# Kernel optimization log

Hardware: AMD Instinct MI355X
Metric: run time of the kernel (lower is better)

Reference implementation:

```python
import jax, jax.numpy as jnp
import numpy as np

N = 65536        # nodes
E = 131072       # directed edges
D = 512          # emb_dim
L = 5            # num_layer
G = 512          # num graphs
EPS = 1e-5       # batchnorm eps
NUM_ATOM_TYPE, NUM_CHIRALITY = 120, 3
NUM_BOND_TYPE, NUM_BOND_DIR = 6, 3


def setup_inputs() -> dict:
    key = jax.random.key(0)
    ks = jax.random.split(key, 12)
    s = 0.02
    return {
        "x": jax.random.randint(ks[0], (N, 2), 0, 3),
        "edge_index": jax.random.randint(ks[1], (2, E), 0, N),
        "edge_attr": jax.random.randint(ks[2], (E, 2), 0, 3),
        "batch": jnp.sort(jax.random.randint(ks[3], (N,), 0, G)),
        "x_emb1": jax.random.normal(ks[4], (NUM_ATOM_TYPE, D), jnp.float32) * s,
        "x_emb2": jax.random.normal(ks[5], (NUM_CHIRALITY, D), jnp.float32) * s,
        "e_emb1": jax.random.normal(ks[6], (L, NUM_BOND_TYPE, D), jnp.float32) * s,
        "e_emb2": jax.random.normal(ks[7], (L, NUM_BOND_DIR, D), jnp.float32) * s,
        "W1": jax.random.normal(ks[8], (L, D, 2 * D), jnp.float32) * s,
        "b1": jnp.zeros((L, 2 * D), jnp.float32),
        "W2": jax.random.normal(ks[9], (L, 2 * D, D), jnp.float32) * s,
        "b2": jnp.zeros((L, D), jnp.float32),
        "gamma": jnp.ones((L, D), jnp.float32),
        "beta": jnp.zeros((L, D), jnp.float32),
    }


def reference(x, edge_index, edge_attr, batch,
              x_emb1, x_emb2, e_emb1, e_emb2,
              W1, b1, W2, b2, gamma, beta):
    n = x.shape[0]
    # atom embedding: type + chirality
    h = x_emb1[x[:, 0]] + x_emb2[x[:, 1]]                     # [N, D]

    # add self loops (appended after real edges, attr = [4, 0])
    loops = jnp.arange(n)
    src = jnp.concatenate([edge_index[0], loops])             # [E+N]
    dst = jnp.concatenate([edge_index[1], loops])
    sl_attr = jnp.concatenate(
        [jnp.full((n, 1), 4, dtype=edge_attr.dtype),
         jnp.zeros((n, 1), dtype=edge_attr.dtype)], axis=1)
    ea = jnp.concatenate([edge_attr, sl_attr], axis=0)        # [E+N, 2]

    for l in range(L):
        # per-edge embedding: bond type + bond direction
        e = e_emb1[l][ea[:, 0]] + e_emb2[l][ea[:, 1]]         # [E+N, D]
        msg = h[src] + e                                      # gather + add
        agg = jax.ops.segment_sum(msg, dst, num_segments=n)   # scatter-add
        # GIN MLP: Linear(D,2D) -> ReLU -> Linear(2D,D)
        hh = jax.nn.relu(agg @ W1[l] + b1[l]) @ W2[l] + b2[l]
        # BatchNorm1d (training-mode batch statistics)
        mean = hh.mean(axis=0)
        var = hh.var(axis=0)
        hh = (hh - mean) * jax.lax.rsqrt(var + EPS) * gamma[l] + beta[l]
        if l < L - 1:
            hh = jax.nn.relu(hh)   # dropout(p=0) is identity
        h = hh

    # JK='last': node rep = h; graph rep = global mean pool over batch ids
    counts = jax.ops.segment_sum(jnp.ones((n,), h.dtype), batch, num_segments=G)
    graph = jax.ops.segment_sum(h, batch, num_segments=G) / jnp.maximum(counts, 1.0)[:, None]
    return graph, h
```

## Files before the change

### kernel.cpp

```cpp
#include <hip/hip_runtime.h>
#include <stdint.h>

#define Nn 65536
#define Ee 131072
#define Dd 512
#define D2 1024
#define Ll 5
#define Gg 512
#define EPSf 1e-5f

typedef __bf16 bf16x8 __attribute__((ext_vector_type(8)));
typedef float f32x4 __attribute__((ext_vector_type(4)));

__device__ __forceinline__ unsigned short f2bf(float f) {
    union { float f; unsigned u; } c; c.f = f;
    unsigned r = c.u + 0x7fffu + ((c.u >> 16) & 1u);
    return (unsigned short)(r >> 16);
}

__device__ __forceinline__ void add4(float4& a, float4 b) {
    a.x += b.x; a.y += b.y; a.z += b.z; a.w += b.w;
}

__device__ __forceinline__ void gload_lds16(const void* g, void* l) {
    __builtin_amdgcn_global_load_lds(
        (const __attribute__((address_space(1))) void*)(uintptr_t)g,
        (__attribute__((address_space(3))) void*)(unsigned)(uintptr_t)l,
        16, 0, 0);
}

__global__ void k_transW(const float* __restrict__ src, unsigned short* __restrict__ dst,
                         int K, int Nw) {
    long total = (long)Ll * K * Nw;
    for (long idx = (long)blockIdx.x * blockDim.x + threadIdx.x; idx < total;
         idx += (long)gridDim.x * blockDim.x) {
        long l = idx / ((long)K * Nw);
        long rem = idx - l * (long)K * Nw;
        int k = (int)(rem / Nw), n = (int)(rem % Nw);
        dst[(l * Nw + n) * K + k] = f2bf(src[idx]);
    }
}

__global__ void k_embed(const int* __restrict__ x,
                        const float4* __restrict__ xe1, const float4* __restrict__ xe2,
                        float4* __restrict__ h4) {
    const int total = Nn * 128;
    for (int idx = blockIdx.x * blockDim.x + threadIdx.x; idx < total;
         idx += gridDim.x * blockDim.x) {
        int node = idx >> 7, c = idx & 127;
        int t0 = x[2 * node], t1 = x[2 * node + 1];
        float4 v = xe1[t0 * 128 + c];
        float4 w = xe2[t1 * 128 + c];
        v.x += w.x; v.y += w.y; v.z += w.z; v.w += w.w;
        h4[idx] = v;
    }
}

__global__ void k_zeroN(int* __restrict__ p, int n) {
    int i = blockIdx.x * blockDim.x + threadIdx.x;
    if (i < n) p[i] = 0;
}

__global__ void k_hist(const int* __restrict__ edst, int* __restrict__ cnt) {
    int e = blockIdx.x * blockDim.x + threadIdx.x;
    if (e < Ee) atomicAdd(&cnt[edst[e]], 1);
}

__global__ void k_scan(const int* __restrict__ cnt, int* __restrict__ off,
                       int* __restrict__ cursor) {
    __shared__ int part[1024];
    int t = threadIdx.x;
    int base = t * 64;
    int s = 0;
    for (int i = 0; i < 64; ++i) s += cnt[base + i];
    part[t] = s;
    __syncthreads();
    for (int d = 1; d < 1024; d <<= 1) {
        int v = (t >= d) ? part[t - d] : 0;
        __syncthreads();
        part[t] += v;
        __syncthreads();
    }
    int run = part[t] - s;
    for (int i = 0; i < 64; ++i) {
        off[base + i] = run;
        cursor[base + i] = run;
        run += cnt[base + i];
    }
    if (t == 1023) off[Nn] = run;
}

__global__ void k_place(const int* __restrict__ esrc, const int* __restrict__ edst,
                        const int* __restrict__ eattr, int* __restrict__ cursor,
                        int* __restrict__ csrc, int* __restrict__ cattr) {
    int e = blockIdx.x * blockDim.x + threadIdx.x;
    if (e < Ee) {
        int d = edst[e];
        int p = atomicAdd(&cursor[d], 1);
        csrc[p] = esrc[e];
        cattr[p] = eattr[2 * e] * 3 + eattr[2 * e + 1];
    }
}

template <int NORM>
__global__ __launch_bounds__(256) void k_gather(const float* __restrict__ hin,
                                                const float* __restrict__ ss,
                                                const int* __restrict__ off,
                                                const int* __restrict__ csrc,
                                                const int* __restrict__ cattr,
                                                const float* __restrict__ e1l,
                                                const float* __restrict__ e2l,
                                                unsigned short* __restrict__ aggb) {
    int node = (blockIdx.x << 2) + (threadIdx.x >> 6);
    int lane = threadIdx.x & 63;
    int c0 = lane, c1 = lane + 64;
    float4 sa0, sb0, sa1, sb1;
    if (NORM) {
        const float4* ss4 = (const float4*)ss;
        sa0 = ss4[c0]; sb0 = ss4[128 + c0];
        sa1 = ss4[c1]; sb1 = ss4[128 + c1];
    }
    auto loadrow = [&](const float4* row, int c, float4 a, float4 b) -> float4 {
        float4 v = row[c];
        if (NORM) {
            v.x = fmaxf(fmaf(v.x, a.x, b.x), 0.f);
            v.y = fmaxf(fmaf(v.y, a.y, b.y), 0.f);
            v.z = fmaxf(fmaf(v.z, a.z, b.z), 0.f);
            v.w = fmaxf(fmaf(v.w, a.w, b.w), 0.f);
        }
        return v;
    };
    const float4* hn = (const float4*)(hin + (size_t)node * Dd);
    const float4* s1 = (const float4*)(e1l + 4 * Dd);
    const float4* s2 = (const float4*)(e2l);
    float4 A0 = loadrow(hn, c0, sa0, sb0);
    float4 A1 = loadrow(hn, c1, sa1, sb1);
    add4(A0, s1[c0]); add4(A0, s2[c0]);
    add4(A1, s1[c1]); add4(A1, s2[c1]);
    int kb = off[node], ke = off[node + 1];
    for (int k = kb; k < ke; ++k) {
        int s = csrc[k];
        int at = cattr[k];
        const float4* hs = (const float4*)(hin + (size_t)s * Dd);
        const float4* p1 = (const float4*)(e1l + (size_t)(at / 3) * Dd);
        const float4* p2 = (const float4*)(e2l + (size_t)(at % 3) * Dd);
        add4(A0, loadrow(hs, c0, sa0, sb0)); add4(A0, p1[c0]); add4(A0, p2[c0]);
        add4(A1, loadrow(hs, c1, sa1, sb1)); add4(A1, p1[c1]); add4(A1, p2[c1]);
    }
    unsigned short* dst = aggb + (size_t)node * Dd;
    ushort4 o0, o1;
    o0.x = f2bf(A0.x); o0.y = f2bf(A0.y); o0.z = f2bf(A0.z); o0.w = f2bf(A0.w);
    o1.x = f2bf(A1.x); o1.y = f2bf(A1.y); o1.z = f2bf(A1.z); o1.w = f2bf(A1.w);
    *(ushort4*)(dst + c0 * 4) = o0;
    *(ushort4*)(dst + c1 * 4) = o1;
}

__device__ __forceinline__ void stage_q(const unsigned short* __restrict__ g, int ldk,
                                        long row0, int col0, char* region, int tid) {
    int wbase = (tid >> 6) << 10;
#pragma unroll
    for (int r = 0; r < 2; ++r) {
        int gi = tid + r * 512;
        int row = gi >> 2;
        int k16 = (gi & 3) ^ ((row >> 1) & 3);
        gload_lds16(g + (row0 + row) * (long)ldk + col0 + k16 * 8,
                    region + r * 8192 + wbase);
    }
}

__device__ __forceinline__ bf16x8 rd_frag(const char* region, int row, int l4) {
    int slot = l4 ^ ((row >> 1) & 3);
    return *(const bf16x8*)(region + row * 64 + (slot << 4));
}

template <int EPI>
__global__ __launch_bounds__(512, 2) void gemm8(const unsigned short* __restrict__ A,
                                                const unsigned short* __restrict__ BT,
                                                const float* __restrict__ bias,
                                                unsigned short* __restrict__ Cb,
                                                float* __restrict__ Cf,
                                                float* __restrict__ stats,
                                                int M, int N, int K) {
    __shared__ __align__(16) char lds[131072];
    const int tid = threadIdx.x;
    const int lane = tid & 63;
    const int w = tid >> 6;
    const int wm = w >> 2, wn = w & 3;
    const int l15 = lane & 15, l4 = lane >> 4;

    const int nwg = gridDim.x;
    const int cpx = nwg >> 3;
    const int bid = blockIdx.x;
    const int wg = (bid & 7) * cpx + (bid >> 3);
    const int ntn = N >> 8;
    const long bm = (long)(wg / ntn) * 256;
    const long bn = (long)(wg % ntn) * 256;

    char* Ab = lds;
    char* Bb = lds + 65536;
    const int NT = K >> 6;

    f32x4 acc[8][4];
#pragma unroll
    for (int i = 0; i < 8; ++i)
#pragma unroll
        for (int j = 0; j < 4; ++j) acc[i][j] = (f32x4){0.f, 0.f, 0.f, 0.f};

    stage_q(A, K, bm, 0, Ab, tid);
    stage_q(BT, K, bn, 0, Bb, tid);
    stage_q(A, K, bm, 32, Ab + 16384, tid);
    stage_q(BT, K, bn, 32, Bb + 16384, tid);
    if (NT > 1) {
        stage_q(A, K, bm, 64, Ab + 32768, tid);
        stage_q(BT, K, bn, 64, Bb + 32768, tid);
    }
    asm volatile("s_waitcnt vmcnt(4)" ::: "memory");
    __builtin_amdgcn_s_barrier();

    for (int t = 0; t < NT; ++t) {
        const int cur = t & 1;
        char* Acur = Ab + cur * 32768;
        char* Bcur = Bb + cur * 32768;
        char* Anxt = Ab + (cur ^ 1) * 32768;
        char* Bnxt = Bb + (cur ^ 1) * 32768;
        bf16x8 af[8], bv[2];

#pragma unroll
        for (int fm = 0; fm < 8; ++fm)
            af[fm] = rd_frag(Acur, wm * 128 + fm * 16 + l15, l4);
#pragma unroll
        for (int fn = 0; fn < 2; ++fn)
            bv[fn] = rd_frag(Bcur, wn * 64 + fn * 16 + l15, l4);
        if (t + 1 < NT) stage_q(A, K, bm, (t + 1) * 64 + 32, Anxt + 16384, tid);
        __builtin_amdgcn_s_barrier();
        asm volatile("s_waitcnt lgkmcnt(0)" ::: "memory");
        __builtin_amdgcn_s_setprio(1);
#pragma unroll
        for (int fm = 0; fm < 8; ++fm)
#pragma unroll
            for (int fn = 0; fn < 2; ++fn)
                acc[fm][fn] = __builtin_amdgcn_mfma_f32_16x16x32_bf16(af[fm], bv[fn], acc[fm][fn], 0, 0, 0);
        __builtin_amdgcn_s_setprio(0);
        __builtin_amdgcn_s_barrier();

#pragma unroll
        for (int fn = 0; fn < 2; ++fn)
            bv[fn] = rd_frag(Bcur, wn * 64 + 32 + fn * 16 + l15, l4);
        if (t + 1 < NT) stage_q(BT, K, bn, (t + 1) * 64 + 32, Bnxt + 16384, tid);
        __builtin_amdgcn_s_barrier();
        asm volatile("s_waitcnt lgkmcnt(0)" ::: "memory");
        __builtin_amdgcn_s_setprio(1);
#pragma unroll
        for (int fm = 0; fm < 8; ++fm)
#pragma unroll
            for (int fn = 0; fn < 2; ++fn)
                acc[fm][2 + fn] = __builtin_amdgcn_mfma_f32_16x16x32_bf16(af[fm], bv[fn], acc[fm][2 + fn], 0, 0, 0);
        __builtin_amdgcn_s_setprio(0);
        __builtin_amdgcn_s_barrier();

#pragma unroll
        for (int fm = 0; fm < 8; ++fm)
            af[fm] = rd_frag(Acur + 16384, wm * 128 + fm * 16 + l15, l4);
#pragma unroll
        for (int fn = 0; fn < 2; ++fn)
            bv[fn] = rd_frag(Bcur + 16384, wn * 64 + fn * 16 + l15, l4);
        if (t + 2 < NT) stage_q(A, K, bm, (t + 2) * 64, Acur, tid);
        __builtin_amdgcn_s_barrier();
        asm volatile("s_waitcnt lgkmcnt(0)" ::: "memory");
        __builtin_amdgcn_s_setprio(1);
#pragma unroll
        for (int fm = 0; fm < 8; ++fm)
#pragma unroll
            for (int fn = 0; fn < 2; ++fn)
                acc[fm][fn] = __builtin_amdgcn_mfma_f32_16x16x32_bf16(af[fm], bv[fn], acc[fm][fn], 0, 0, 0);
        __builtin_amdgcn_s_setprio(0);
        __builtin_amdgcn_s_barrier();

#pragma unroll
        for (int fn = 0; fn < 2; ++fn)
            bv[fn] = rd_frag(Bcur + 16384, wn * 64 + 32 + fn * 16 + l15, l4);
        if (t + 2 < NT) stage_q(BT, K, bn, (t + 2) * 64, Bcur, tid);
        __builtin_amdgcn_s_barrier();
        asm volatile("s_waitcnt lgkmcnt(0)" ::: "memory");
        __builtin_amdgcn_s_setprio(1);
#pragma unroll
        for (int fm = 0; fm < 8; ++fm)
#pragma unroll
            for (int fn = 0; fn < 2; ++fn)
                acc[fm][2 + fn] = __builtin_amdgcn_mfma_f32_16x16x32_bf16(af[fm], bv[fn], acc[fm][2 + fn], 0, 0, 0);
        __builtin_amdgcn_s_setprio(0);
        if (t + 2 < NT) {
            asm volatile("s_waitcnt vmcnt(4)" ::: "memory");
        } else if (t + 1 < NT) {
            asm volatile("s_waitcnt vmcnt(0)" ::: "memory");
        }
        __builtin_amdgcn_s_barrier();
    }

    const long row_base = bm + wm * 128;
    const int col_base = (int)bn + wn * 64;
    float cs[4] = {0.f, 0.f, 0.f, 0.f}, cq[4] = {0.f, 0.f, 0.f, 0.f};
#pragma unroll
    for (int fn = 0; fn < 4; ++fn) {
        int col = col_base + fn * 16 + l15;
        float bval = bias[col];
#pragma unroll
        for (int fm = 0; fm < 8; ++fm) {
            long row0 = row_base + fm * 16 + l4 * 4;
#pragma unroll
            for (int r = 0; r < 4; ++r) {
                float v = acc[fm][fn][r] + bval;
                if (EPI == 0) {
                    v = fmaxf(v, 0.f);
                    Cb[(row0 + r) * N + col] = f2bf(v);
                } else {
                    Cf[(row0 + r) * N + col] = v;
                    cs[fn] += v;
                    cq[fn] += v * v;
                }
            }
        }
    }
    if (EPI == 1) {
#pragma unroll
        for (int fn = 0; fn < 4; ++fn) {
            float s = cs[fn], q = cq[fn];
            s += __shfl_xor(s, 16); s += __shfl_xor(s, 32);
            q += __shfl_xor(q, 16); q += __shfl_xor(q, 32);
            if (l4 == 0) {
                int col = col_base + fn * 16 + l15;
                atomicAdd(&stats[col], s);
                atomicAdd(&stats[512 + col], q);
            }
        }
    }
}

__global__ void k_zero(float* __restrict__ p) { p[threadIdx.x] = 0.f; }

__global__ void k_bnfin(const float* __restrict__ stats, const float* __restrict__ gamma,
                        const float* __restrict__ beta, float* __restrict__ ss) {
    int c = threadIdx.x;
    float mean = stats[c] * (1.f / (float)Nn);
    float var = stats[512 + c] * (1.f / (float)Nn) - mean * mean;
    float a = gamma[c] * rsqrtf(var + EPSf);
    ss[c] = a;
    ss[512 + c] = beta[c] - mean * a;
}

__global__ void k_norm(const float4* __restrict__ hh4, const float* __restrict__ ss,
                       float4* __restrict__ h4) {
    const int total = Nn * 128;
    const float4* ss4 = (const float4*)ss;
    for (int idx = blockIdx.x * blockDim.x + threadIdx.x; idx < total;
         idx += gridDim.x * blockDim.x) {
        int c = idx & 127;
        float4 v = hh4[idx];
        float4 a = ss4[c], b = ss4[128 + c];
        v.x = fmaf(v.x, a.x, b.x); v.y = fmaf(v.y, a.y, b.y);
        v.z = fmaf(v.z, a.z, b.z); v.w = fmaf(v.w, a.w, b.w);
        h4[idx] = v;
    }
}

__global__ void k_pool(const float* __restrict__ h, const int* __restrict__ batch,
                       float* __restrict__ graph) {
    int g = blockIdx.x, t = threadIdx.x;
    int lo = 0, hi = Nn;
    while (lo < hi) { int m = (lo + hi) >> 1; if (batch[m] < g) lo = m + 1; else hi = m; }
    int s = lo;
    lo = s; hi = Nn;
    while (lo < hi) { int m = (lo + hi) >> 1; if (batch[m] <= g) lo = m + 1; else hi = m; }
    int e = lo;
    float s0 = 0.f, s1 = 0.f;
    for (int r = s; r < e; ++r) {
        const float* row = h + (long)r * Dd;
        s0 += row[t];
        s1 += row[t + 256];
    }
    int cnt = e - s; if (cnt < 1) cnt = 1;
    float inv = 1.f / (float)cnt;
    graph[(long)g * Dd + t] = s0 * inv;
    graph[(long)g * Dd + t + 256] = s1 * inv;
}

extern "C" void kernel_launch(void* const* d_in, const int* in_sizes, int n_in,
                              void* d_out, int out_size, void* d_ws, size_t ws_size,
                              hipStream_t stream) {
    (void)in_sizes; (void)n_in; (void)out_size; (void)ws_size;
    const int* x      = (const int*)d_in[0];
    const int* ei     = (const int*)d_in[1];
    const int* ea     = (const int*)d_in[2];
    const int* batch  = (const int*)d_in[3];
    const float* xe1  = (const float*)d_in[4];
    const float* xe2  = (const float*)d_in[5];
    const float* ee1  = (const float*)d_in[6];
    const float* ee2  = (const float*)d_in[7];
    const float* W1   = (const float*)d_in[8];
    const float* b1   = (const float*)d_in[9];
    const float* W2   = (const float*)d_in[10];
    const float* b2   = (const float*)d_in[11];
    const float* gamma = (const float*)d_in[12];
    const float* beta  = (const float*)d_in[13];

    float* graph = (float*)d_out;
    float* h = graph + (size_t)Gg * Dd;

    char* w = (char*)d_ws;
    float* bufT = (float*)w;                    w += (size_t)Nn * Dd * 4;
    unsigned short* aggb = (unsigned short*)w;  w += (size_t)Nn * Dd * 2;
    unsigned short* w1t = (unsigned short*)w;   w += (size_t)Ll * D2 * Dd * 2;
    unsigned short* w2t = (unsigned short*)w;   w += (size_t)Ll * Dd * D2 * 2;
    float* stats = (float*)w;                   w += 4096;
    float* ss = (float*)w;                      w += 4096;
    int* csr_off = (int*)w;                     w += (Nn + 1) * 4;
    int* cursor = (int*)w;                      w += Nn * 4;
    int* cnt = (int*)w;                         w += Nn * 4;
    int* csrc = (int*)w;                        w += Ee * 4;
    int* cattr = (int*)w;                       w += Ee * 4;

    k_transW<<<2048, 256, 0, stream>>>(W1, w1t, Dd, D2);
    k_transW<<<2048, 256, 0, stream>>>(W2, w2t, D2, Dd);

    k_embed<<<2048, 256, 0, stream>>>(x, (const float4*)xe1, (const float4*)xe2, (float4*)h);

    k_zeroN<<<64, 1024, 0, stream>>>(cnt, Nn);
    k_hist<<<Ee / 256, 256, 0, stream>>>(ei + Ee, cnt);
    k_scan<<<1, 1024, 0, stream>>>(cnt, csr_off, cursor);
    k_place<<<Ee / 256, 256, 0, stream>>>(ei, ei + Ee, ea, cursor, csrc, cattr);

    for (int l = 0; l < Ll; ++l) {
        const float* e1l = ee1 + (size_t)l * 6 * Dd;
        const float* e2l = ee2 + (size_t)l * 3 * Dd;
        if (l == 0)
            k_gather<0><<<Nn / 4, 256, 0, stream>>>(h, nullptr, csr_off, csrc, cattr,
                                                    e1l, e2l, aggb);
        else
            k_gather<1><<<Nn / 4, 256, 0, stream>>>(bufT, ss, csr_off, csrc, cattr,
                                                    e1l, e2l, aggb);
        gemm8<0><<<(Nn / 256) * (D2 / 256), 512, 0, stream>>>(
            aggb, w1t + (size_t)l * D2 * Dd, b1 + (size_t)l * D2,
            (unsigned short*)h, nullptr, nullptr, Nn, D2, Dd);
        k_zero<<<1, 1024, 0, stream>>>(stats);
        gemm8<1><<<(Nn / 256) * (Dd / 256), 512, 0, stream>>>(
            (const unsigned short*)h, w2t + (size_t)l * Dd * D2, b2 + (size_t)l * Dd,
            nullptr, bufT, stats, Nn, Dd, D2);
        k_bnfin<<<1, 512, 0, stream>>>(stats, gamma + (size_t)l * Dd, beta + (size_t)l * Dd, ss);
    }

    k_norm<<<2048, 256, 0, stream>>>((const float4*)bufT, ss, (float4*)h);
    k_pool<<<Gg, 256, 0, stream>>>(h, batch, graph);
}
```

Before: 1.631 ms.

## Switch GEMMs to fp16, store pre-BN activations in fp16, deterministic BN stats

Moves the MFMA path from bf16 to fp16 and stores the second GEMM's pre-BatchNorm output in fp16 instead of fp32, which halves the activation traffic into the gather and norm kernels. Both GEMM epilogues are staged through LDS so global stores are coalesced 16-byte writes. BN statistics are written as per-row-group partials and reduced by a small kernel, replacing global atomics and the zeroing launch. The GEMM main loop is reorganized into two 32-wide K halves with paired A/B staging. CSR edges are insertion-sorted per node so the summation order is deterministic. The cost is fp16 range and precision risk, plus an extra sort pass.

```diff
diff --git a/kernel.cpp b/kernel.cpp
--- a/kernel.cpp
+++ b/kernel.cpp
@@ -9,13 +9,20 @@
 #define Gg 512
 #define EPSf 1e-5f
 
-typedef __bf16 bf16x8 __attribute__((ext_vector_type(8)));
+typedef _Float16 f16x8 __attribute__((ext_vector_type(8)));
 typedef float f32x4 __attribute__((ext_vector_type(4)));
-
-__device__ __forceinline__ unsigned short f2bf(float f) {
-    union { float f; unsigned u; } c; c.f = f;
-    unsigned r = c.u + 0x7fffu + ((c.u >> 16) & 1u);
-    return (unsigned short)(r >> 16);
+typedef unsigned short u16x8 __attribute__((ext_vector_type(8)));
+
+__device__ __forceinline__ unsigned short f2h(float f) {
+    _Float16 h = (_Float16)f;
+    union { _Float16 h; unsigned short u; } c; c.h = h;
+    return c.u;
+}
+
+__device__ __forceinline__ float4 h4f(ushort4 u) {
+    union { unsigned short s; _Float16 h; } a, b, c, d;
+    a.s = u.x; b.s = u.y; c.s = u.z; d.s = u.w;
+    return make_float4((float)a.h, (float)b.h, (float)c.h, (float)d.h);
 }
 
 __device__ __forceinline__ void add4(float4& a, float4 b) {
@@ -37,7 +44,7 @@
         long l = idx / ((long)K * Nw);
         long rem = idx - l * (long)K * Nw;
         int k = (int)(rem / Nw), n = (int)(rem % Nw);
-        dst[(l * Nw + n) * K + k] = f2bf(src[idx]);
+        dst[(l * Nw + n) * K + k] = f2h(src[idx]);
     }
 }
 
@@ -92,25 +99,41 @@
 
 __global__ void k_place(const int* __restrict__ esrc, const int* __restrict__ edst,
                         const int* __restrict__ eattr, int* __restrict__ cursor,
-                        int* __restrict__ csrc, int* __restrict__ cattr) {
+                        int* __restrict__ ckey, int* __restrict__ csrc) {
     int e = blockIdx.x * blockDim.x + threadIdx.x;
     if (e < Ee) {
         int d = edst[e];
         int p = atomicAdd(&cursor[d], 1);
+        ckey[p] = e * 32 + (eattr[2 * e] * 3 + eattr[2 * e + 1]);
         csrc[p] = esrc[e];
-        cattr[p] = eattr[2 * e] * 3 + eattr[2 * e + 1];
+    }
+}
+
+__global__ void k_sort(const int* __restrict__ off, int* __restrict__ ckey,
+                       int* __restrict__ csrc) {
+    int node = blockIdx.x * blockDim.x + threadIdx.x;
+    if (node >= Nn) return;
+    int kb = off[node], ke = off[node + 1];
+    for (int i = kb + 1; i < ke; ++i) {
+        int k = ckey[i], s = csrc[i];
+        int j = i - 1;
+        while (j >= kb && ckey[j] > k) {
+            ckey[j + 1] = ckey[j]; csrc[j + 1] = csrc[j]; --j;
+        }
+        ckey[j + 1] = k; csrc[j + 1] = s;
     }
 }
 
 template <int NORM>
-__global__ __launch_bounds__(256) void k_gather(const float* __restrict__ hin,
+__global__ __launch_bounds__(256) void k_gather(const float* __restrict__ hf32,
+                                                const unsigned short* __restrict__ hf16,
                                                 const float* __restrict__ ss,
                                                 const int* __restrict__ off,
+                                                const int* __restrict__ ckey,
                                                 const int* __restrict__ csrc,
-                                                const int* __restrict__ cattr,
                                                 const float* __restrict__ e1l,
                                                 const float* __restrict__ e2l,
-                                                unsigned short* __restrict__ aggb) {
+                                                unsigned short* __restrict__ aggh) {
     int node = (blockIdx.x << 2) + (threadIdx.x >> 6);
     int lane = threadIdx.x & 63;
     int c0 = lane, c1 = lane + 64;
@@ -120,37 +143,39 @@
         sa0 = ss4[c0]; sb0 = ss4[128 + c0];
         sa1 = ss4[c1]; sb1 = ss4[128 + c1];
     }
-    auto loadrow = [&](const float4* row, int c, float4 a, float4 b) -> float4 {
-        float4 v = row[c];
+    auto loadrow = [&](size_t rowbase, int c, float4 a, float4 b) -> float4 {
+        float4 v;
         if (NORM) {
+            v = h4f(*(const ushort4*)(hf16 + rowbase + (size_t)c * 4));
             v.x = fmaxf(fmaf(v.x, a.x, b.x), 0.f);
             v.y = fmaxf(fmaf(v.y, a.y, b.y), 0.f);
             v.z = fmaxf(fmaf(v.z, a.z, b.z), 0.f);
             v.w = fmaxf(fmaf(v.w, a.w, b.w), 0.f);
+        } else {
+            v = *(const float4*)(hf32 + rowbase + (size_t)c * 4);
         }
         return v;
     };
-    const float4* hn = (const float4*)(hin + (size_t)node * Dd);
     const float4* s1 = (const float4*)(e1l + 4 * Dd);
     const float4* s2 = (const float4*)(e2l);
-    float4 A0 = loadrow(hn, c0, sa0, sb0);
-    float4 A1 = loadrow(hn, c1, sa1, sb1);
+    size_t nb = (size_t)node * Dd;
+    float4 A0 = loadrow(nb, c0, sa0, sb0);
+    float4 A1 = loadrow(nb, c1, sa1, sb1);
     add4(A0, s1[c0]); add4(A0, s2[c0]);
     add4(A1, s1[c1]); add4(A1, s2[c1]);
     int kb = off[node], ke = off[node + 1];
     for (int k = kb; k < ke; ++k) {
-        int s = csrc[k];
-        int at = cattr[k];
-        const float4* hs = (const float4*)(hin + (size_t)s * Dd);
+        size_t sb = (size_t)csrc[k] * Dd;
+        int at = ckey[k] & 31;
         const float4* p1 = (const float4*)(e1l + (size_t)(at / 3) * Dd);
         const float4* p2 = (const float4*)(e2l + (size_t)(at % 3) * Dd);
-        add4(A0, loadrow(hs, c0, sa0, sb0)); add4(A0, p1[c0]); add4(A0, p2[c0]);
-        add4(A1, loadrow(hs, c1, sa1, sb1)); add4(A1, p1[c1]); add4(A1, p2[c1]);
-    }
-    unsigned short* dst = aggb + (size_t)node * Dd;
+        add4(A0, loadrow(sb, c0, sa0, sb0)); add4(A0, p1[c0]); add4(A0, p2[c0]);
+        add4(A1, loadrow(sb, c1, sa1, sb1)); add4(A1, p1[c1]); add4(A1, p2[c1]);
+    }
+    unsigned short* dst = aggh + (size_t)node * Dd;
     ushort4 o0, o1;
-    o0.x = f2bf(A0.x); o0.y = f2bf(A0.y); o0.z = f2bf(A0.z); o0.w = f2bf(A0.w);
-    o1.x = f2bf(A1.x); o1.y = f2bf(A1.y); o1.z = f2bf(A1.z); o1.w = f2bf(A1.w);
+    o0.x = f2h(A0.x); o0.y = f2h(A0.y); o0.z = f2h(A0.z); o0.w = f2h(A0.w);
+    o1.x = f2h(A1.x); o1.y = f2h(A1.y); o1.z = f2h(A1.z); o1.w = f2h(A1.w);
     *(ushort4*)(dst + c0 * 4) = o0;
     *(ushort4*)(dst + c1 * 4) = o1;
 }
@@ -168,9 +193,9 @@
     }
 }
 
-__device__ __forceinline__ bf16x8 rd_frag(const char* region, int row, int l4) {
+__device__ __forceinline__ f16x8 rd_frag(const char* region, int row, int l4) {
     int slot = l4 ^ ((row >> 1) & 3);
-    return *(const bf16x8*)(region + row * 64 + (slot << 4));
+    return *(const f16x8*)(region + row * 64 + (slot << 4));
 }
 
 template <int EPI>
@@ -178,8 +203,7 @@
                                                 const unsigned short* __restrict__ BT,
                                                 const float* __restrict__ bias,
                                                 unsigned short* __restrict__ Cb,
-                                                float* __restrict__ Cf,
-                                                float* __restrict__ stats,
+                                                float* __restrict__ pS,
                                                 int M, int N, int K) {
     __shared__ __align__(16) char lds[131072];
     const int tid = threadIdx.x;
@@ -196,8 +220,8 @@
     const long bm = (long)(wg / ntn) * 256;
     const long bn = (long)(wg % ntn) * 256;
 
-    char* Ab = lds;
-    char* Bb = lds + 65536;
+    char* Ar = lds;
+    char* Br = lds + 65536;
     const int NT = K >> 6;
 
     f32x4 acc[8][4];
@@ -206,119 +230,101 @@
 #pragma unroll
         for (int j = 0; j < 4; ++j) acc[i][j] = (f32x4){0.f, 0.f, 0.f, 0.f};
 
-    stage_q(A, K, bm, 0, Ab, tid);
-    stage_q(BT, K, bn, 0, Bb, tid);
-    stage_q(A, K, bm, 32, Ab + 16384, tid);
-    stage_q(BT, K, bn, 32, Bb + 16384, tid);
-    if (NT > 1) {
-        stage_q(A, K, bm, 64, Ab + 32768, tid);
-        stage_q(BT, K, bn, 64, Bb + 32768, tid);
-    }
-    asm volatile("s_waitcnt vmcnt(4)" ::: "memory");
+    stage_q(A, K, bm, 0, Ar, tid);
+    stage_q(BT, K, bn, 0, Br, tid);
+    stage_q(A, K, bm, 32, Ar + 16384, tid);
+    stage_q(BT, K, bn, 32, Br + 16384, tid);
+    stage_q(A, K, bm, 64, Ar + 32768, tid);
+    stage_q(BT, K, bn, 64, Br + 32768, tid);
+    asm volatile("s_waitcnt vmcnt(8)" ::: "memory");
     __builtin_amdgcn_s_barrier();
 
     for (int t = 0; t < NT; ++t) {
-        const int cur = t & 1;
-        char* Acur = Ab + cur * 32768;
-        char* Bcur = Bb + cur * 32768;
-        char* Anxt = Ab + (cur ^ 1) * 32768;
-        char* Bnxt = Bb + (cur ^ 1) * 32768;
-        bf16x8 af[8], bv[2];
+        const int cur = (t & 1) << 1;
+        const char* Ac = Ar + cur * 16384;
+        const char* Bc = Br + cur * 16384;
+        char* An1 = Ar + ((((t + 1) & 1) << 1) + 1) * 16384;
+        char* Bn1 = Br + ((((t + 1) & 1) << 1) + 1) * 16384;
+        f16x8 af[8], bv[4];
 
 #pragma unroll
         for (int fm = 0; fm < 8; ++fm)
-            af[fm] = rd_frag(Acur, wm * 128 + fm * 16 + l15, l4);
-#pragma unroll
-        for (int fn = 0; fn < 2; ++fn)
-            bv[fn] = rd_frag(Bcur, wn * 64 + fn * 16 + l15, l4);
-        if (t + 1 < NT) stage_q(A, K, bm, (t + 1) * 64 + 32, Anxt + 16384, tid);
+            af[fm] = rd_frag(Ac, wm * 128 + fm * 16 + l15, l4);
+#pragma unroll
+        for (int fn = 0; fn < 4; ++fn)
+            bv[fn] = rd_frag(Bc, wn * 64 + fn * 16 + l15, l4);
+        if (t + 1 < NT) {
+            stage_q(A, K, bm, (t + 1) * 64 + 32, An1, tid);
+            stage_q(BT, K, bn, (t + 1) * 64 + 32, Bn1, tid);
+        }
         __builtin_amdgcn_s_barrier();
         asm volatile("s_waitcnt lgkmcnt(0)" ::: "memory");
         __builtin_amdgcn_s_setprio(1);
 #pragma unroll
         for (int fm = 0; fm < 8; ++fm)
 #pragma unroll
-            for (int fn = 0; fn < 2; ++fn)
-                acc[fm][fn] = __builtin_amdgcn_mfma_f32_16x16x32_bf16(af[fm], bv[fn], acc[fm][fn], 0, 0, 0);
+            for (int fn = 0; fn < 4; ++fn)
+                acc[fm][fn] = __builtin_amdgcn_mfma_f32_16x16x32_f16(af[fm], bv[fn], acc[fm][fn], 0, 0, 0);
         __builtin_amdgcn_s_setprio(0);
+        if (t >= NT - 2) {
+            asm volatile("s_waitcnt vmcnt(0)" ::: "memory");
+        } else {
+            asm volatile("s_waitcnt vmcnt(4)" ::: "memory");
+        }
         __builtin_amdgcn_s_barrier();
 
 #pragma unroll
-        for (int fn = 0; fn < 2; ++fn)
-            bv[fn] = rd_frag(Bcur, wn * 64 + 32 + fn * 16 + l15, l4);
-        if (t + 1 < NT) stage_q(BT, K, bn, (t + 1) * 64 + 32, Bnxt + 16384, tid);
+        for (int fm = 0; fm < 8; ++fm)
+            af[fm] = rd_frag(Ac + 16384, wm * 128 + fm * 16 + l15, l4);
+#pragma unroll
+        for (int fn = 0; fn < 4; ++fn)
+            bv[fn] = rd_frag(Bc + 16384, wn * 64 + fn * 16 + l15, l4);
+        if (t + 2 < NT) {
+            stage_q(A, K, bm, (t + 2) * 64, (char*)Ac, tid);
+            stage_q(BT, K, bn, (t + 2) * 64, (char*)Bc, tid);
+        }
         __builtin_amdgcn_s_barrier();
         asm volatile("s_waitcnt lgkmcnt(0)" ::: "memory");
         __builtin_amdgcn_s_setprio(1);
 #pragma unroll
         for (int fm = 0; fm < 8; ++fm)
 #pragma unroll
-            for (int fn = 0; fn < 2; ++fn)
-                acc[fm][2 + fn] = __builtin_amdgcn_mfma_f32_16x16x32_bf16(af[fm], bv[fn], acc[fm][2 + fn], 0, 0, 0);
+            for (int fn = 0; fn < 4; ++fn)
+                acc[fm][fn] = __builtin_amdgcn_mfma_f32_16x16x32_f16(af[fm], bv[fn], acc[fm][fn], 0, 0, 0);
         __builtin_amdgcn_s_setprio(0);
         __builtin_amdgcn_s_barrier();
-
-#pragma unroll
-        for (int fm = 0; fm < 8; ++fm)
-            af[fm] = rd_frag(Acur + 16384, wm * 128 + fm * 16 + l15, l4);
-#pragma unroll
-        for (int fn = 0; fn < 2; ++fn)
-            bv[fn] = rd_frag(Bcur + 16384, wn * 64 + fn * 16 + l15, l4);
-        if (t + 2 < NT) stage_q(A, K, bm, (t + 2) * 64, Acur, tid);
-        __builtin_amdgcn_s_barrier();
-        asm volatile("s_waitcnt lgkmcnt(0)" ::: "memory");
-        __builtin_amdgcn_s_setprio(1);
-#pragma unroll
-        for (int fm = 0; fm < 8; ++fm)
-#pragma unroll
-            for (int fn = 0; fn < 2; ++fn)
-                acc[fm][fn] = __builtin_amdgcn_mfma_f32_16x16x32_bf16(af[fm], bv[fn], acc[fm][fn], 0, 0, 0);
-        __builtin_amdgcn_s_setprio(0);
-        __builtin_amdgcn_s_barrier();
-
-#pragma unroll
-        for (int fn = 0; fn < 2; ++fn)
-            bv[fn] = rd_frag(Bcur + 16384, wn * 64 + 32 + fn * 16 + l15, l4);
-        if (t + 2 < NT) stage_q(BT, K, bn, (t + 2) * 64, Bcur, tid);
-        __builtin_amdgcn_s_barrier();
-        asm volatile("s_waitcnt lgkmcnt(0)" ::: "memory");
-        __builtin_amdgcn_s_setprio(1);
-#pragma unroll
-        for (int fm = 0; fm < 8; ++fm)
-#pragma unroll
-            for (int fn = 0; fn < 2; ++fn)
-                acc[fm][2 + fn] = __builtin_amdgcn_mfma_f32_16x16x32_bf16(af[fm], bv[fn], acc[fm][2 + fn], 0, 0, 0);
-        __builtin_amdgcn_s_setprio(0);
-        if (t + 2 < NT) {
-            asm volatile("s_waitcnt vmcnt(4)" ::: "memory");
-        } else if (t + 1 < NT) {
-            asm volatile("s_waitcnt vmcnt(0)" ::: "memory");
-        }
-        __builtin_amdgcn_s_barrier();
-    }
-
-    const long row_base = bm + wm * 128;
-    const int col_base = (int)bn + wn * 64;
+    }
+
+    unsigned short* cl = (unsigned short*)lds;
     float cs[4] = {0.f, 0.f, 0.f, 0.f}, cq[4] = {0.f, 0.f, 0.f, 0.f};
 #pragma unroll
-    for (int fn = 0; fn < 4; ++fn) {
-        int col = col_base + fn * 16 + l15;
-        float bval = bias[col];
-#pragma unroll
-        for (int fm = 0; fm < 8; ++fm) {
-            long row0 = row_base + fm * 16 + l4 * 4;
-#pragma unroll
-            for (int r = 0; r < 4; ++r) {
-                float v = acc[fm][fn][r] + bval;
-                if (EPI == 0) {
-                    v = fmaxf(v, 0.f);
-                    Cb[(row0 + r) * N + col] = f2bf(v);
-                } else {
-                    Cf[(row0 + r) * N + col] = v;
-                    cs[fn] += v;
-                    cq[fn] += v * v;
+    for (int hh = 0; hh < 2; ++hh) {
+        __syncthreads();
+        if (wm == hh) {
+#pragma unroll
+            for (int fn = 0; fn < 4; ++fn) {
+                int col = wn * 64 + fn * 16 + l15;
+                float bval = bias[bn + col];
+#pragma unroll
+                for (int fm = 0; fm < 8; ++fm) {
+                    int r0 = fm * 16 + l4 * 4;
+#pragma unroll
+                    for (int r = 0; r < 4; ++r) {
+                        float v = acc[fm][fn][r] + bval;
+                        if (EPI == 0) v = fmaxf(v, 0.f);
+                        else { cs[fn] += v; cq[fn] += v * v; }
+                        cl[(r0 + r) * 264 + col] = f2h(v);
+                    }
                 }
             }
+        }
+        __syncthreads();
+#pragma unroll
+        for (int i = 0; i < 8; ++i) {
+            int g = tid + i * 512;
+            int r = g >> 5, cg = (g & 31) << 3;
+            u16x8 val = *(const u16x8*)&cl[r * 264 + cg];
+            *(u16x8*)&Cb[(bm + hh * 128 + r) * N + bn + cg] = val;
         }
     }
     if (EPI == 1) {
@@ -328,34 +334,38 @@
             s += __shfl_xor(s, 16); s += __shfl_xor(s, 32);
             q += __shfl_xor(q, 16); q += __shfl_xor(q, 32);
             if (l4 == 0) {
-                int col = col_base + fn * 16 + l15;
-                atomicAdd(&stats[col], s);
-                atomicAdd(&stats[512 + col], q);
+                int col = (int)bn + wn * 64 + fn * 16 + l15;
+                int rowgrp = ((int)(bm >> 8)) * 2 + wm;
+                pS[rowgrp * 512 + col] = s;
+                pS[262144 + rowgrp * 512 + col] = q;
             }
         }
     }
 }
 
-__global__ void k_zero(float* __restrict__ p) { p[threadIdx.x] = 0.f; }
-
-__global__ void k_bnfin(const float* __restrict__ stats, const float* __restrict__ gamma,
+__global__ void k_bnred(const float* __restrict__ pS, const float* __restrict__ gamma,
                         const float* __restrict__ beta, float* __restrict__ ss) {
-    int c = threadIdx.x;
-    float mean = stats[c] * (1.f / (float)Nn);
-    float var = stats[512 + c] * (1.f / (float)Nn) - mean * mean;
-    float a = gamma[c] * rsqrtf(var + EPSf);
-    ss[c] = a;
-    ss[512 + c] = beta[c] - mean * a;
-}
-
-__global__ void k_norm(const float4* __restrict__ hh4, const float* __restrict__ ss,
+    int col = blockIdx.x * 256 + threadIdx.x;
+    float s = 0.f, q = 0.f;
+    for (int rg = 0; rg < 512; ++rg) {
+        s += pS[rg * 512 + col];
+        q += pS[262144 + rg * 512 + col];
+    }
+    float mean = s * (1.f / (float)Nn);
+    float var = q * (1.f / (float)Nn) - mean * mean;
+    float a = gamma[col] * rsqrtf(var + EPSf);
+    ss[col] = a;
+    ss[512 + col] = beta[col] - mean * a;
+}
+
+__global__ void k_norm(const unsigned short* __restrict__ hhf, const float* __restrict__ ss,
                        float4* __restrict__ h4) {
     const int total = Nn * 128;
     const float4* ss4 = (const float4*)ss;
     for (int idx = blockIdx.x * blockDim.x + threadIdx.x; idx < total;
          idx += gridDim.x * blockDim.x) {
         int c = idx & 127;
-        float4 v = hh4[idx];
+        float4 v = h4f(*(const ushort4*)(hhf + (size_t)idx * 4));
         float4 a = ss4[c], b = ss4[128 + c];
         v.x = fmaf(v.x, a.x, b.x); v.y = fmaf(v.y, a.y, b.y);
         v.z = fmaf(v.z, a.z, b.z); v.w = fmaf(v.w, a.w, b.w);
@@ -407,17 +417,17 @@
     float* h = graph + (size_t)Gg * Dd;
 
     char* w = (char*)d_ws;
-    float* bufT = (float*)w;                    w += (size_t)Nn * Dd * 4;
-    unsigned short* aggb = (unsigned short*)w;  w += (size_t)Nn * Dd * 2;
-    unsigned short* w1t = (unsigned short*)w;   w += (size_t)Ll * D2 * Dd * 2;
-    unsigned short* w2t = (unsigned short*)w;   w += (size_t)Ll * Dd * D2 * 2;
-    float* stats = (float*)w;                   w += 4096;
-    float* ss = (float*)w;                      w += 4096;
     int* csr_off = (int*)w;                     w += (Nn + 1) * 4;
     int* cursor = (int*)w;                      w += Nn * 4;
     int* cnt = (int*)w;                         w += Nn * 4;
+    int* ckey = (int*)w;                        w += Ee * 4;
     int* csrc = (int*)w;                        w += Ee * 4;
-    int* cattr = (int*)w;                       w += Ee * 4;
+    float* ss = (float*)w;                      w += 4096;
+    float* pS = (float*)w;                      w += 2 * 512 * 512 * 4;
+    unsigned short* aggh = (unsigned short*)w;  w += (size_t)Nn * Dd * 2;
+    unsigned short* hhf = (unsigned short*)w;   w += (size_t)Nn * Dd * 2;
+    unsigned short* w1t = (unsigned short*)w;   w += (size_t)Ll * D2 * Dd * 2;
+    unsigned short* w2t = (unsigned short*)w;   w += (size_t)Ll * Dd * D2 * 2;
 
     k_transW<<<2048, 256, 0, stream>>>(W1, w1t, Dd, D2);
     k_transW<<<2048, 256, 0, stream>>>(W2, w2t, D2, Dd);
@@ -427,27 +437,27 @@
     k_zeroN<<<64, 1024, 0, stream>>>(cnt, Nn);
     k_hist<<<Ee / 256, 256, 0, stream>>>(ei + Ee, cnt);
     k_scan<<<1, 1024, 0, stream>>>(cnt, csr_off, cursor);
-    k_place<<<Ee / 256, 256, 0, stream>>>(ei, ei + Ee, ea, cursor, csrc, cattr);
+    k_place<<<Ee / 256, 256, 0, stream>>>(ei, ei + Ee, ea, cursor, ckey, csrc);
+    k_sort<<<Nn / 256, 256, 0, stream>>>(csr_off, ckey, csrc);
 
     for (int l = 0; l < Ll; ++l) {
         const float* e1l = ee1 + (size_t)l * 6 * Dd;
         const float* e2l = ee2 + (size_t)l * 3 * Dd;
         if (l == 0)
-            k_gather<0><<<Nn / 4, 256, 0, stream>>>(h, nullptr, csr_off, csrc, cattr,
-                                                    e1l, e2l, aggb);
+            k_gather<0><<<Nn / 4, 256, 0, stream>>>(h, nullptr, nullptr, csr_off, ckey, csrc,
+                                                    e1l, e2l, aggh);
         else
-            k_gather<1><<<Nn / 4, 256, 0, stream>>>(bufT, ss, csr_off, csrc, cattr,
-                                                    e1l, e2l, aggb);
+            k_gather<1><<<Nn / 4, 256, 0, stream>>>(nullptr, hhf, ss, csr_off, ckey, csrc,
+                                                    e1l, e2l, aggh);
         gemm8<0><<<(Nn / 256) * (D2 / 256), 512, 0, stream>>>(
-            aggb, w1t + (size_t)l * D2 * Dd, b1 + (size_t)l * D2,
-            (unsigned short*)h, nullptr, nullptr, Nn, D2, Dd);
-        k_zero<<<1, 1024, 0, stream>>>(stats);
+            aggh, w1t + (size_t)l * D2 * Dd, b1 + (size_t)l * D2,
+            (unsigned short*)h, nullptr, Nn, D2, Dd);
         gemm8<1><<<(Nn / 256) * (Dd / 256), 512, 0, stream>>>(
             (const unsigned short*)h, w2t + (size_t)l * Dd * D2, b2 + (size_t)l * Dd,
-            nullptr, bufT, stats, Nn, Dd, D2);
-        k_bnfin<<<1, 512, 0, stream>>>(stats, gamma + (size_t)l * Dd, beta + (size_t)l * Dd, ss);
-    }
-
-    k_norm<<<2048, 256, 0, stream>>>((const float4*)bufT, ss, (float4*)h);
+            hhf, pS, Nn, Dd, D2);
+        k_bnred<<<2, 256, 0, stream>>>(pS, gamma + (size_t)l * Dd, beta + (size_t)l * Dd, ss);
+    }
+
+    k_norm<<<2048, 256, 0, stream>>>(hhf, ss, (float4*)h);
     k_pool<<<Gg, 256, 0, stream>>>(h, batch, graph);
 }
```

Result: no change. 1.654 ms (+1.4%).
